# Kernel tuning notes

Hardware: AMD Instinct MI355X
Metric: run time of the kernel (lower is better)

The kernel has to match this reference:

```python
import jax, jax.numpy as jnp
import numpy as np
import math

HEAD_DIM = 128

def _rope(t, cos, sin):
    # t: [B, S, H, D]; cos/sin: [S, D//2]; rotates consecutive pairs (view_as_complex semantics)
    B, S, H, D = t.shape
    t2 = t.reshape(B, S, H, D // 2, 2)
    t0, t1 = t2[..., 0], t2[..., 1]
    c = cos[None, :, None, :]
    s = sin[None, :, None, :]
    r0 = t0 * c - t1 * s
    r1 = t0 * s + t1 * c
    return jnp.stack([r0, r1], axis=-1).reshape(B, S, H, D)

def setup_inputs() -> dict:
    key = jax.random.key(0)
    ks = jax.random.split(key, 8)
    B, S, dim = 32, 1, 4096
    n_q, n_kv, hd = 32, 8, HEAD_DIM
    max_seq = 2048
    start_pos = 2047
    x = jax.random.normal(ks[0], (B, S, dim), dtype=jnp.float32)
    wq = jax.random.normal(ks[1], (n_q * hd, dim), dtype=jnp.float32) * 0.02
    wk = jax.random.normal(ks[2], (n_kv * hd, dim), dtype=jnp.float32) * 0.02
    wv = jax.random.normal(ks[3], (n_kv * hd, dim), dtype=jnp.float32) * 0.02
    wo = jax.random.normal(ks[4], (dim, n_q * hd), dtype=jnp.float32) * 0.02
    # real RoPE frequencies at positions [start_pos, start_pos+S)
    inv_freq = 1.0 / (10000.0 ** (np.arange(0, hd, 2, dtype=np.float32) / hd))  # [hd//2]
    pos = np.arange(start_pos, start_pos + S, dtype=np.float32)[:, None]
    angles = pos * inv_freq[None, :]  # [S, hd//2]
    freqs_cos = jnp.asarray(np.cos(angles), dtype=jnp.float32)
    freqs_sin = jnp.asarray(np.sin(angles), dtype=jnp.float32)
    cache_k = jax.random.normal(ks[5], (B, max_seq, n_kv, hd), dtype=jnp.float32)
    cache_v = jax.random.normal(ks[6], (B, max_seq, n_kv, hd), dtype=jnp.float32)
    return {"x": x, "wq": wq, "wk": wk, "wv": wv, "wo": wo,
            "freqs_cos": freqs_cos, "freqs_sin": freqs_sin,
            "cache_k": cache_k, "cache_v": cache_v, "start_pos": start_pos}

def reference(x, wq, wk, wv, wo, freqs_cos, freqs_sin, cache_k, cache_v, start_pos):
    B, S, dim = x.shape
    hd = HEAD_DIM
    n_q = wq.shape[0] // hd
    n_kv = wk.shape[0] // hd
    rep = n_q // n_kv
    q = (x @ wq.T).reshape(B, S, n_q, hd)
    k = (x @ wk.T).reshape(B, S, n_kv, hd)
    v = (x @ wv.T).reshape(B, S, n_kv, hd)
    q = _rope(q, freqs_cos, freqs_sin)
    k = _rope(k, freqs_cos, freqs_sin)
    # KV-cache update (start_pos is a static Python int)
    ck = jax.lax.dynamic_update_slice(cache_k, k, (0, start_pos, 0, 0))
    cv = jax.lax.dynamic_update_slice(cache_v, v, (0, start_pos, 0, 0))
    T = start_pos + S
    kk = ck[:, :T]  # [B, T, n_kv, hd]
    vv = cv[:, :T]
    # GQA without materializing repeated heads: q head h -> (g=h//rep, r=h%rep)
    qg = q.reshape(B, S, n_kv, rep, hd)
    scores = jnp.einsum('bsgrd,btgd->bgrst', qg, kk) / math.sqrt(hd)
    attn = jax.nn.softmax(scores, axis=-1)
    out = jnp.einsum('bgrst,btgd->bsgrd', attn, vv).reshape(B, S, n_q * hd)
    return out @ wo.T
```

## Files before the change

### kernel.cpp

```cpp
#include <hip/hip_runtime.h>
#include <hip/hip_bf16.h>


typedef __bf16 bf16x8_t __attribute__((ext_vector_type(8)));
typedef float f32x4_t __attribute__((ext_vector_type(4)));

#define KDIM 4096
#define NTOT_QKV 6144
#define NTOT_O 4096
#define NKV 8
#define HD 128
#define TCHUNK 256

static __device__ inline bf16x8_t cvt8(const float4* p) {
  float4 u = p[0], v = p[1];
  bf16x8_t r;
  r[0] = (__bf16)u.x; r[1] = (__bf16)u.y; r[2] = (__bf16)u.z; r[3] = (__bf16)u.w;
  r[4] = (__bf16)v.x; r[5] = (__bf16)v.y; r[6] = (__bf16)v.z; r[7] = (__bf16)v.w;
  return r;
}

__global__ __launch_bounds__(256) void qkv_mfma(
    const float* __restrict__ X,
    const float* __restrict__ Wq,
    const float* __restrict__ Wk,
    const float* __restrict__ Wv,
    float* __restrict__ part)
{
  int wid  = (blockIdx.x * blockDim.x + threadIdx.x) >> 6;
  int lane = threadIdx.x & 63;
  const int ntiles = NTOT_QKV >> 4;
  int nt = wid % ntiles;
  int kc = wid / ntiles;
  int k0 = kc << 9;
  int rr = lane & 15;
  int quad = lane >> 4;

  int ng = nt * 16 + rr;
  const float* Wrow;
  if (ng < 4096)      Wrow = Wq + (size_t)ng * KDIM;
  else if (ng < 5120) Wrow = Wk + (size_t)(ng - 4096) * KDIM;
  else                Wrow = Wv + (size_t)(ng - 5120) * KDIM;

  const float4* pa0 = (const float4*)(X + (size_t)rr * KDIM + k0) + quad * 2;
  const float4* pa1 = (const float4*)(X + (size_t)(rr + 16) * KDIM + k0) + quad * 2;
  const float4* pbv = (const float4*)(Wrow + k0) + quad * 2;

  f32x4_t acc0 = {0.f, 0.f, 0.f, 0.f};
  f32x4_t acc1 = {0.f, 0.f, 0.f, 0.f};
  #pragma unroll 4
  for (int s = 0; s < 16; ++s) {
    bf16x8_t a0 = cvt8(pa0 + s * 8);
    bf16x8_t a1 = cvt8(pa1 + s * 8);
    bf16x8_t bb = cvt8(pbv + s * 8);
    acc0 = __builtin_amdgcn_mfma_f32_16x16x32_bf16(a0, bb, acc0, 0, 0, 0);
    acc1 = __builtin_amdgcn_mfma_f32_16x16x32_bf16(a1, bb, acc1, 0, 0, 0);
  }
  float* p = part + (size_t)kc * 32 * NTOT_QKV + ng;
  #pragma unroll
  for (int i = 0; i < 4; ++i) {
    int m = quad * 4 + i;
    p[(size_t)m * NTOT_QKV] = acc0[i];
    p[(size_t)(m + 16) * NTOT_QKV] = acc1[i];
  }
}

__global__ __launch_bounds__(256) void reduce_rope(
    const float* __restrict__ part,
    const float* __restrict__ cosv,
    const float* __restrict__ sinv,
    float* __restrict__ qws,
    float* __restrict__ kws,
    float* __restrict__ vws)
{
  int idx = blockIdx.x * blockDim.x + threadIdx.x;
  int b = idx / 3072;
  int rem = idx - b * 3072;
  int n0 = rem * 2;
  const float* p = part + (size_t)b * NTOT_QKV + n0;
  float s0 = 0.f, s1 = 0.f;
  #pragma unroll
  for (int c = 0; c < 8; ++c) {
    s0 += p[(size_t)c * 32 * NTOT_QKV + 0];
    s1 += p[(size_t)c * 32 * NTOT_QKV + 1];
  }
  if (n0 < 4096) {
    int d = n0 & 127; int j = d >> 1;
    float cf = cosv[j], sf = sinv[j];
    qws[(size_t)b * 4096 + n0]     = s0 * cf - s1 * sf;
    qws[(size_t)b * 4096 + n0 + 1] = s0 * sf + s1 * cf;
  } else if (n0 < 5120) {
    int nn = n0 - 4096;
    int d = nn & 127; int j = d >> 1;
    float cf = cosv[j], sf = sinv[j];
    kws[(size_t)b * 1024 + nn]     = s0 * cf - s1 * sf;
    kws[(size_t)b * 1024 + nn + 1] = s0 * sf + s1 * cf;
  } else {
    int nn = n0 - 5120;
    vws[(size_t)b * 1024 + nn]     = s0;
    vws[(size_t)b * 1024 + nn + 1] = s1;
  }
}

__global__ __launch_bounds__(256) void attn_partial(
    const float* __restrict__ cache_k,
    const float* __restrict__ cache_v,
    const float* __restrict__ qws,
    const float* __restrict__ kws,
    const float* __restrict__ vws,
    float* __restrict__ part)
{
  int bidx = blockIdx.x;
  int c = bidx & 7;
  int pair = bidx >> 3;
  int h = pair & 7, b = pair >> 3;
  int tid = threadIdx.x;

  __shared__ float q_lds[512];
  __shared__ float p_lds[4 * TCHUNK];
  __shared__ float mred4[16];
  __shared__ float lred4[16];

  q_lds[tid]       = qws[(size_t)b * 4096 + h * 512 + tid];
  q_lds[tid + 256] = qws[(size_t)b * 4096 + h * 512 + 256 + tid];
  __syncthreads();

  int t = c * TCHUNK + tid;
  float s[4] = {0.f, 0.f, 0.f, 0.f};

  const float* kp = cache_k + (((size_t)b * 2048 + t) * NKV + h) * HD;
  #pragma unroll 4
  for (int dc = 0; dc < HD; dc += 8) {
    float4 ka = *(const float4*)(kp + dc);
    float4 kb = *(const float4*)(kp + dc + 4);
    #pragma unroll
    for (int r = 0; r < 4; ++r) {
      const float4 qa = *(const float4*)(q_lds + r * HD + dc);
      const float4 qb = *(const float4*)(q_lds + r * HD + dc + 4);
      s[r] += ka.x*qa.x + ka.y*qa.y + ka.z*qa.z + ka.w*qa.w
            + kb.x*qb.x + kb.y*qb.y + kb.z*qb.z + kb.w*qb.w;
    }
  }
  if (t == 2047) {
    #pragma unroll
    for (int r = 0; r < 4; ++r) s[r] = 0.f;
    const float* kn = kws + ((size_t)b * NKV + h) * HD;
    for (int dc = 0; dc < HD; dc += 4) {
      float4 k4 = *(const float4*)(kn + dc);
      #pragma unroll
      for (int r = 0; r < 4; ++r) {
        const float* qr = q_lds + r * HD + dc;
        s[r] += k4.x*qr[0] + k4.y*qr[1] + k4.z*qr[2] + k4.w*qr[3];
      }
    }
  }
  const float scale = 0.088388347648318447f;
  #pragma unroll
  for (int r = 0; r < 4; ++r) s[r] *= scale;

  int lane = tid & 63, wv = tid >> 6;
  float m[4];
  #pragma unroll
  for (int r = 0; r < 4; ++r) {
    float mx = s[r];
    for (int off = 32; off; off >>= 1) mx = fmaxf(mx, __shfl_xor(mx, off, 64));
    if (lane == 0) mred4[r * 4 + wv] = mx;
  }
  __syncthreads();
  #pragma unroll
  for (int r = 0; r < 4; ++r)
    m[r] = fmaxf(fmaxf(mred4[r*4], mred4[r*4+1]), fmaxf(mred4[r*4+2], mred4[r*4+3]));

  #pragma unroll
  for (int r = 0; r < 4; ++r) {
    float pv = __expf(s[r] - m[r]);
    p_lds[r * TCHUNK + tid] = pv;
    float sm = pv;
    for (int off = 32; off; off >>= 1) sm += __shfl_xor(sm, off, 64);
    if (lane == 0) lred4[r * 4 + wv] = sm;
  }
  __syncthreads();
  float l[4];
  #pragma unroll
  for (int r = 0; r < 4; ++r)
    l[r] = lred4[r*4] + lred4[r*4+1] + lred4[r*4+2] + lred4[r*4+3];

  int r0 = tid >> 7;
  int d = tid & 127;
  const float* vp = cache_v + (((size_t)b * 2048 + c * TCHUNK) * NKV + h) * HD + d;
  float acc0 = 0.f, acc1 = 0.f;
  #pragma unroll 4
  for (int tt = 0; tt < TCHUNK; ++tt) {
    float v = vp[(size_t)tt * (NKV * HD)];
    acc0 += p_lds[r0 * TCHUNK + tt] * v;
    acc1 += p_lds[(r0 + 2) * TCHUNK + tt] * v;
  }
  if (c == 7) {
    const float* vn = vws + ((size_t)b * NKV + h) * HD + d;
    float vc = vp[(size_t)255 * (NKV * HD)];
    float dv = vn[0] - vc;
    acc0 += p_lds[r0 * TCHUNK + 255] * dv;
    acc1 += p_lds[(r0 + 2) * TCHUNK + 255] * dv;
  }

  float* pb = part + (size_t)bidx * 520;
  pb[8 + r0 * 128 + d] = acc0;
  pb[8 + (r0 + 2) * 128 + d] = acc1;
  if (tid == 0) {
    #pragma unroll
    for (int r = 0; r < 4; ++r) { pb[r] = m[r]; pb[4 + r] = l[r]; }
  }
}

__global__ __launch_bounds__(128) void attn_combine(
    const float* __restrict__ part,
    float* __restrict__ attn_out)
{
  int pair = blockIdx.x;
  int h = pair & 7, b = pair >> 3;
  int d = threadIdx.x;
  const float* pb = part + (size_t)pair * 8 * 520;
  #pragma unroll
  for (int r = 0; r < 4; ++r) {
    float M = -1e30f;
    #pragma unroll
    for (int c = 0; c < 8; ++c) M = fmaxf(M, pb[c * 520 + r]);
    float L = 0.f, o = 0.f;
    #pragma unroll
    for (int c = 0; c < 8; ++c) {
      float w = __expf(pb[c * 520 + r] - M);
      L += w * pb[c * 520 + 4 + r];
      o += w * pb[c * 520 + 8 + r * 128 + d];
    }
    attn_out[(size_t)b * 4096 + (h * 4 + r) * 128 + d] = o / L;
  }
}

__global__ __launch_bounds__(256) void oproj_mfma(
    const float* __restrict__ X,
    const float* __restrict__ W,
    float* __restrict__ part)
{
  int wid  = (blockIdx.x * blockDim.x + threadIdx.x) >> 6;
  int lane = threadIdx.x & 63;
  const int ntiles = NTOT_O >> 4;
  int nt = wid % ntiles;
  int kc = wid / ntiles;
  int k0 = kc << 9;
  int rr = lane & 15;
  int quad = lane >> 4;
  int ng = nt * 16 + rr;

  const float4* pa0 = (const float4*)(X + (size_t)rr * KDIM + k0) + quad * 2;
  const float4* pa1 = (const float4*)(X + (size_t)(rr + 16) * KDIM + k0) + quad * 2;
  const float4* pbv = (const float4*)(W + (size_t)ng * KDIM + k0) + quad * 2;

  f32x4_t acc0 = {0.f, 0.f, 0.f, 0.f};
  f32x4_t acc1 = {0.f, 0.f, 0.f, 0.f};
  #pragma unroll 4
  for (int s = 0; s < 16; ++s) {
    bf16x8_t a0 = cvt8(pa0 + s * 8);
    bf16x8_t a1 = cvt8(pa1 + s * 8);
    bf16x8_t bb = cvt8(pbv + s * 8);
    acc0 = __builtin_amdgcn_mfma_f32_16x16x32_bf16(a0, bb, acc0, 0, 0, 0);
    acc1 = __builtin_amdgcn_mfma_f32_16x16x32_bf16(a1, bb, acc1, 0, 0, 0);
  }
  float* p = part + (size_t)kc * 32 * NTOT_O + ng;
  #pragma unroll
  for (int i = 0; i < 4; ++i) {
    int m = quad * 4 + i;
    p[(size_t)m * NTOT_O] = acc0[i];
    p[(size_t)(m + 16) * NTOT_O] = acc1[i];
  }
}

__global__ __launch_bounds__(256) void oproj_reduce(
    const float* __restrict__ part,
    float* __restrict__ out)
{
  int i = blockIdx.x * blockDim.x + threadIdx.x;
  float s = 0.f;
  #pragma unroll
  for (int c = 0; c < 8; ++c) s += part[(size_t)c * 131072 + i];
  out[i] = s;
}

extern "C" void kernel_launch(void* const* d_in, const int* in_sizes, int n_in,
                              void* d_out, int out_size, void* d_ws, size_t ws_size,
                              hipStream_t stream) {
  const float* x  = (const float*)d_in[0];
  const float* wq = (const float*)d_in[1];
  const float* wk = (const float*)d_in[2];
  const float* wv = (const float*)d_in[3];
  const float* wo = (const float*)d_in[4];
  const float* fc = (const float*)d_in[5];
  const float* fs = (const float*)d_in[6];
  const float* ck = (const float*)d_in[7];
  const float* cv = (const float*)d_in[8];

  char* ws = (char*)d_ws;
  float* part_qkv = (float*)(ws + 0);
  float* qws      = (float*)(ws + 6291456);
  float* kws      = (float*)(ws + 6815744);
  float* vws      = (float*)(ws + 6946816);
  float* part_at  = (float*)(ws + 7077888);
  float* attn_out = (float*)(ws + 11337728);
  float* part_o   = (float*)(ws + 0);

  qkv_mfma<<<768, 256, 0, stream>>>(x, wq, wk, wv, part_qkv);
  reduce_rope<<<384, 256, 0, stream>>>(part_qkv, fc, fs, qws, kws, vws);
  attn_partial<<<2048, 256, 0, stream>>>(ck, cv, qws, kws, vws, part_at);
  attn_combine<<<256, 128, 0, stream>>>(part_at, attn_out);
  oproj_mfma<<<512, 256, 0, stream>>>(attn_out, wo, part_o);
  oproj_reduce<<<512, 256, 0, stream>>>(part_o, (float*)d_out);
}
```

Measured before the change: 724.6 us.

## Stage K tiles through swizzled LDS and vectorize attention partial loads

```diff
diff --git a/kernel.cpp b/kernel.cpp
--- a/kernel.cpp
+++ b/kernel.cpp
@@ -10,7 +10,6 @@
 #define NTOT_O 4096
 #define NKV 8
 #define HD 128
-#define TCHUNK 256
 
 static __device__ inline bf16x8_t cvt8(const float4* p) {
   float4 u = p[0], v = p[1];
@@ -116,99 +115,111 @@
   int h = pair & 7, b = pair >> 3;
   int tid = threadIdx.x;
 
-  __shared__ float q_lds[512];
-  __shared__ float p_lds[4 * TCHUNK];
-  __shared__ float mred4[16];
-  __shared__ float lred4[16];
-
-  q_lds[tid]       = qws[(size_t)b * 4096 + h * 512 + tid];
-  q_lds[tid + 256] = qws[(size_t)b * 4096 + h * 512 + 256 + tid];
+  __shared__ float4 kbuf[2048];
+  __shared__ float4 q4l[128];
+  __shared__ float4 pl4[256];
+
+  if (tid < 128)
+    q4l[tid] = ((const float4*)(qws + (size_t)b * 4096 + (size_t)h * 512))[tid];
+
+  const int r  = tid >> 6;
+  const int tl = tid & 63;
+  const int sw = tl & 7;
+
+  float s[4];
+  #pragma unroll
+  for (int st = 0; st < 4; ++st) {
+    int t0 = c * 256 + st * 64;
+    float4 tmp[8];
+    #pragma unroll
+    for (int j = 0; j < 8; ++j) {
+      int f = tid + j * 256;
+      int row = f >> 5, col = f & 31;
+      const float4* src;
+      if (c == 7 && st == 3 && row == 63)
+        src = (const float4*)(kws + ((size_t)b * NKV + h) * HD) + col;
+      else
+        src = (const float4*)(cache_k + (((size_t)b * 2048 + t0 + row) * NKV + h) * HD) + col;
+      tmp[j] = *src;
+    }
+    #pragma unroll
+    for (int j = 0; j < 8; ++j) {
+      int f = tid + j * 256;
+      int row = f >> 5, col = f & 31;
+      kbuf[row * 32 + (col ^ (row & 7))] = tmp[j];
+    }
+    __syncthreads();
+    const float4* kr = kbuf + tl * 32;
+    float acc = 0.f;
+    #pragma unroll 8
+    for (int d4 = 0; d4 < 32; ++d4) {
+      float4 q4 = q4l[r * 32 + d4];
+      float4 k4 = kr[d4 ^ sw];
+      acc += q4.x * k4.x + q4.y * k4.y + q4.z * k4.z + q4.w * k4.w;
+    }
+    s[st] = acc * 0.088388347648318447f;
+    __syncthreads();
+  }
+
+  float m = fmaxf(fmaxf(s[0], s[1]), fmaxf(s[2], s[3]));
+  #pragma unroll
+  for (int off = 32; off; off >>= 1) m = fmaxf(m, __shfl_xor(m, off, 64));
+  float lsum = 0.f;
+  float* plf = (float*)pl4;
+  #pragma unroll
+  for (int st = 0; st < 4; ++st) {
+    float p = __expf(s[st] - m);
+    lsum += p;
+    plf[(st * 64 + tl) * 4 + r] = p;
+  }
+  #pragma unroll
+  for (int off = 32; off; off >>= 1) lsum += __shfl_xor(lsum, off, 64);
+
+  float* pb = part + (size_t)bidx * 520;
+  if (tl == 0) { pb[r] = m; pb[4 + r] = lsum; }
   __syncthreads();
 
-  int t = c * TCHUNK + tid;
-  float s[4] = {0.f, 0.f, 0.f, 0.f};
-
-  const float* kp = cache_k + (((size_t)b * 2048 + t) * NKV + h) * HD;
+  int d4 = tid & 31;
+  int g  = tid >> 3 >> 2;
+  float4 a0 = {0,0,0,0}, a1 = {0,0,0,0}, a2 = {0,0,0,0}, a3 = {0,0,0,0};
+  const float4* vp = (const float4*)(cache_v +
+      (((size_t)b * 2048 + c * 256 + g * 32) * NKV + h) * HD) + d4;
   #pragma unroll 4
-  for (int dc = 0; dc < HD; dc += 8) {
-    float4 ka = *(const float4*)(kp + dc);
-    float4 kb = *(const float4*)(kp + dc + 4);
-    #pragma unroll
-    for (int r = 0; r < 4; ++r) {
-      const float4 qa = *(const float4*)(q_lds + r * HD + dc);
-      const float4 qb = *(const float4*)(q_lds + r * HD + dc + 4);
-      s[r] += ka.x*qa.x + ka.y*qa.y + ka.z*qa.z + ka.w*qa.w
-            + kb.x*qb.x + kb.y*qb.y + kb.z*qb.z + kb.w*qb.w;
-    }
-  }
-  if (t == 2047) {
-    #pragma unroll
-    for (int r = 0; r < 4; ++r) s[r] = 0.f;
-    const float* kn = kws + ((size_t)b * NKV + h) * HD;
-    for (int dc = 0; dc < HD; dc += 4) {
-      float4 k4 = *(const float4*)(kn + dc);
-      #pragma unroll
-      for (int r = 0; r < 4; ++r) {
-        const float* qr = q_lds + r * HD + dc;
-        s[r] += k4.x*qr[0] + k4.y*qr[1] + k4.z*qr[2] + k4.w*qr[3];
-      }
-    }
-  }
-  const float scale = 0.088388347648318447f;
-  #pragma unroll
-  for (int r = 0; r < 4; ++r) s[r] *= scale;
-
-  int lane = tid & 63, wv = tid >> 6;
-  float m[4];
-  #pragma unroll
-  for (int r = 0; r < 4; ++r) {
-    float mx = s[r];
-    for (int off = 32; off; off >>= 1) mx = fmaxf(mx, __shfl_xor(mx, off, 64));
-    if (lane == 0) mred4[r * 4 + wv] = mx;
-  }
+  for (int i = 0; i < 32; ++i) {
+    float4 v4 = vp[(size_t)i * 256];
+    float4 pv = pl4[g * 32 + i];
+    a0.x += pv.x * v4.x; a0.y += pv.x * v4.y; a0.z += pv.x * v4.z; a0.w += pv.x * v4.w;
+    a1.x += pv.y * v4.x; a1.y += pv.y * v4.y; a1.z += pv.y * v4.z; a1.w += pv.y * v4.w;
+    a2.x += pv.z * v4.x; a2.y += pv.z * v4.y; a2.z += pv.z * v4.z; a2.w += pv.z * v4.w;
+    a3.x += pv.w * v4.x; a3.y += pv.w * v4.y; a3.z += pv.w * v4.z; a3.w += pv.w * v4.w;
+  }
+  if (c == 7 && g == 7) {
+    float4 vold = vp[(size_t)31 * 256];
+    float4 vn = ((const float4*)(vws + ((size_t)b * NKV + h) * HD))[d4];
+    float4 dv; dv.x = vn.x - vold.x; dv.y = vn.y - vold.y;
+    dv.z = vn.z - vold.z; dv.w = vn.w - vold.w;
+    float4 pv = pl4[255];
+    a0.x += pv.x * dv.x; a0.y += pv.x * dv.y; a0.z += pv.x * dv.z; a0.w += pv.x * dv.w;
+    a1.x += pv.y * dv.x; a1.y += pv.y * dv.y; a1.z += pv.y * dv.z; a1.w += pv.y * dv.w;
+    a2.x += pv.z * dv.x; a2.y += pv.z * dv.y; a2.z += pv.z * dv.z; a2.w += pv.z * dv.w;
+    a3.x += pv.w * dv.x; a3.y += pv.w * dv.y; a3.z += pv.w * dv.z; a3.w += pv.w * dv.w;
+  }
+  float4* pred = kbuf;
+  pred[(g * 4 + 0) * 32 + d4] = a0;
+  pred[(g * 4 + 1) * 32 + d4] = a1;
+  pred[(g * 4 + 2) * 32 + d4] = a2;
+  pred[(g * 4 + 3) * 32 + d4] = a3;
   __syncthreads();
-  #pragma unroll
-  for (int r = 0; r < 4; ++r)
-    m[r] = fmaxf(fmaxf(mred4[r*4], mred4[r*4+1]), fmaxf(mred4[r*4+2], mred4[r*4+3]));
-
-  #pragma unroll
-  for (int r = 0; r < 4; ++r) {
-    float pv = __expf(s[r] - m[r]);
-    p_lds[r * TCHUNK + tid] = pv;
-    float sm = pv;
-    for (int off = 32; off; off >>= 1) sm += __shfl_xor(sm, off, 64);
-    if (lane == 0) lred4[r * 4 + wv] = sm;
-  }
-  __syncthreads();
-  float l[4];
-  #pragma unroll
-  for (int r = 0; r < 4; ++r)
-    l[r] = lred4[r*4] + lred4[r*4+1] + lred4[r*4+2] + lred4[r*4+3];
-
-  int r0 = tid >> 7;
-  int d = tid & 127;
-  const float* vp = cache_v + (((size_t)b * 2048 + c * TCHUNK) * NKV + h) * HD + d;
-  float acc0 = 0.f, acc1 = 0.f;
-  #pragma unroll 4
-  for (int tt = 0; tt < TCHUNK; ++tt) {
-    float v = vp[(size_t)tt * (NKV * HD)];
-    acc0 += p_lds[r0 * TCHUNK + tt] * v;
-    acc1 += p_lds[(r0 + 2) * TCHUNK + tt] * v;
-  }
-  if (c == 7) {
-    const float* vn = vws + ((size_t)b * NKV + h) * HD + d;
-    float vc = vp[(size_t)255 * (NKV * HD)];
-    float dv = vn[0] - vc;
-    acc0 += p_lds[r0 * TCHUNK + 255] * dv;
-    acc1 += p_lds[(r0 + 2) * TCHUNK + 255] * dv;
-  }
-
-  float* pb = part + (size_t)bidx * 520;
-  pb[8 + r0 * 128 + d] = acc0;
-  pb[8 + (r0 + 2) * 128 + d] = acc1;
-  if (tid == 0) {
-    #pragma unroll
-    for (int r = 0; r < 4; ++r) { pb[r] = m[r]; pb[4 + r] = l[r]; }
+
+  if (tid < 128) {
+    int r2 = tid >> 5, dd = tid & 31;
+    float4 o = {0,0,0,0};
+    #pragma unroll
+    for (int gg = 0; gg < 8; ++gg) {
+      float4 t4 = pred[(gg * 4 + r2) * 32 + dd];
+      o.x += t4.x; o.y += t4.y; o.z += t4.z; o.w += t4.w;
+    }
+    *(float4*)(pb + 8 + r2 * 128 + dd * 4) = o;
   }
 }
 
```

Result: faster. 642.7 us (-11.3%).
